# Performance work log

Measured on AMD Instinct MI355X. Metric: run time of the kernel, lower is better.

## Reference

```python
import jax, jax.numpy as jnp
import numpy as np

# 8-bit signed symmetric quantization grid (bit buffer in the module is set to 8 at runtime)
SAT_MAX = 127.0
SAT_MIN = -127.0


def _squant_stage(rn, re, un, ue, up_p, dn, de, dn_p):
    """One SQuant flip stage over the last axis (vectorized SQuant_func).

    For each row: e = sum(rounding_error); flip round(|e|) elements.
    If e < 0 (under-rounded overall) flip the highest-up-priority elements up,
    else flip the highest-down-priority elements down. The boundary (last,
    lowest-priority flipped) element gets a nonzero priority in the opposite
    direction so the next (coarser) stage can revert it — this reproduces the
    in-place priority update SQuant_func performs after zeroing priorities.
    All tensors have shape [..., K].
    """
    e_sum = jnp.sum(re, axis=-1)                                   # [...]
    n_flip = jnp.round(jnp.abs(e_sum)).astype(jnp.int32)[..., None]  # [...,1]
    flip_up = (e_sum < 0)[..., None]                               # [...,1]
    prio = jnp.where(flip_up, up_p, dn_p)
    order = jnp.argsort(-prio, axis=-1)        # descending priority
    rank = jnp.argsort(order, axis=-1)         # rank[i] = position of i in order
    mask = rank < n_flip                       # elements to flip
    rn2 = jnp.where(mask, jnp.where(flip_up, un, dn), rn)
    re2 = jnp.where(mask, jnp.where(flip_up, ue, de), re)
    # boundary element (rank == n_flip-1) gets opposite-direction priority
    boundary = mask & (rank == (n_flip - 1))
    b_prio = jnp.where(boundary, jnp.abs(re2), 0.0)
    up_p2 = jnp.where(flip_up, jnp.zeros_like(b_prio), b_prio)
    dn_p2 = jnp.where(flip_up, b_prio, jnp.zeros_like(b_prio))
    return rn2, re2, up_p2, dn_p2


def adaptive_round(x, t_min, t_max):
    rn = jnp.round(x)
    re = rn - x
    # up candidates: elements rounded down (re < 0) and not saturated high
    ue = jnp.where((x >= t_max) | (re > 0), 0.0, re)
    up_p = jnp.abs(ue)
    nz_u = ue != 0
    ue = jnp.where(nz_u, ue + 1.0, ue)
    un = jnp.where(nz_u, rn + 1.0, rn)
    # down candidates: elements rounded up (re > 0) and not saturated low
    de = jnp.where((x <= t_min) | (re < 0), 0.0, re)
    dn_p = jnp.abs(de)
    nz_d = de != 0
    de = jnp.where(nz_d, de - 1.0, de)
    dn = jnp.where(nz_d, rn - 1.0, rn)

    OC, IC = x.shape[0], x.shape[1]
    K = x.size // (OC * IC)
    shp_k = (OC, IC, K)         # squant-k: per (oc, ic) kernel row
    rn_k, re_k, up_p_k, dn_p_k = _squant_stage(
        rn.reshape(shp_k), re.reshape(shp_k),
        un.reshape(shp_k), ue.reshape(shp_k), up_p.reshape(shp_k),
        dn.reshape(shp_k), de.reshape(shp_k), dn_p.reshape(shp_k))
    shp_c = (1, OC, IC * K)     # squant-c: per oc channel row
    rn_c, _, _, _ = _squant_stage(
        rn_k.reshape(shp_c), re_k.reshape(shp_c),
        un.reshape(shp_c), ue.reshape(shp_c), up_p_k.reshape(shp_c),
        dn.reshape(shp_c), de.reshape(shp_c), dn_p_k.reshape(shp_c))
    return rn_c.reshape(x.shape)


def setup_inputs() -> dict:
    key = jax.random.key(0)
    tensor = jax.random.normal(key, (1024, 1024, 3, 3), dtype=jnp.float32)
    return {"tensor": tensor}


def reference(tensor) -> jnp.ndarray:
    # symmetric linear quantization params from tensor min/max (weight path)
    max_abs = jnp.maximum(jnp.abs(jnp.max(tensor)), jnp.abs(jnp.min(tensor)))
    scale = max_abs / SAT_MAX                       # element scale
    q = jnp.clip(tensor / scale, SAT_MIN, SAT_MAX)  # linear_quantize
    q = adaptive_round(q, SAT_MIN, SAT_MAX)         # SQuant adaptive rounding
    return q * scale                                # linear_dequantize
```

## Files before the change

### kernel.cpp

```cpp
#include <hip/hip_runtime.h>

#define OC 1024
#define ICN 1024
#define KK 9
#define NELEM (OC * ICN * KK)
#define CH (ICN * KK)
#define CH4 (CH / 4)
#define CHH (CH / 2)
#define CHH4 (CHH / 4)
#define BT 512
#define KMB 1024

__global__ void __launch_bounds__(256) kmax_part(const float* __restrict__ x,
                                                 float* __restrict__ part) {
    __shared__ float s_m[4];
    const int tid = blockIdx.x * 256 + threadIdx.x;
    const int stride = KMB * 256;
    const float4* x4 = (const float4*)x;
    float m = 0.f;
    #pragma unroll
    for (int k = 0; k < 9; ++k) {
        float4 v = x4[tid + k * stride];
        m = fmaxf(m, fmaxf(fmaxf(fabsf(v.x), fabsf(v.y)), fmaxf(fabsf(v.z), fabsf(v.w))));
    }
    #pragma unroll
    for (int off = 32; off > 0; off >>= 1)
        m = fmaxf(m, __shfl_xor(m, off, 64));
    if ((threadIdx.x & 63) == 0) s_m[threadIdx.x >> 6] = m;
    __syncthreads();
    if (threadIdx.x == 0)
        part[blockIdx.x] = fmaxf(fmaxf(s_m[0], s_m[1]), fmaxf(s_m[2], s_m[3]));
}

__global__ void __launch_bounds__(256) kmax_atomic(const float* __restrict__ x,
                                                   unsigned* __restrict__ ws) {
    __shared__ float s_m[4];
    const int tid = blockIdx.x * 256 + threadIdx.x;
    const int stride = KMB * 256;
    const float4* x4 = (const float4*)x;
    float m = 0.f;
    #pragma unroll
    for (int k = 0; k < 9; ++k) {
        float4 v = x4[tid + k * stride];
        m = fmaxf(m, fmaxf(fmaxf(fabsf(v.x), fabsf(v.y)), fmaxf(fabsf(v.z), fabsf(v.w))));
    }
    #pragma unroll
    for (int off = 32; off > 0; off >>= 1)
        m = fmaxf(m, __shfl_xor(m, off, 64));
    if ((threadIdx.x & 63) == 0) s_m[threadIdx.x >> 6] = m;
    __syncthreads();
    if (threadIdx.x == 0) {
        m = fmaxf(fmaxf(s_m[0], s_m[1]), fmaxf(s_m[2], s_m[3]));
        atomicMax(ws, __float_as_uint(m));
    }
}

template <int C>
__device__ __forceinline__ void red_step(unsigned& key, unsigned& row) {
    unsigned k2 = (unsigned)__builtin_amdgcn_update_dpp(0, (int)key, C, 0xF, 0xF, false);
    unsigned r2 = (unsigned)__builtin_amdgcn_update_dpp(0, (int)row, C, 0xF, 0xF, false);
    if (k2 >= key) { key = k2; row = r2; }
}

__device__ __forceinline__ void wave_argmax(unsigned& key, unsigned& row) {
    red_step<0x111>(key, row);
    red_step<0x112>(key, row);
    red_step<0x114>(key, row);
    red_step<0x118>(key, row);
    red_step<0x142>(key, row);
    red_step<0x143>(key, row);
}

__global__ void __launch_bounds__(BT, 8) squant_kernel(const float* __restrict__ x,
                                                       float* __restrict__ out,
                                                       const float* __restrict__ part,
                                                       int nparts) {
    __shared__ __align__(16) signed char s_q[CH];
    __shared__ __align__(16) float s_stage[CHH];
    __shared__ float s_res[ICN];
    __shared__ float s_prio[ICN];
    __shared__ int   s_meta[ICN];
    __shared__ float s_mx[8];

    const int oc = blockIdx.x;
    const int t  = threadIdx.x;
    const long long ocbase = (long long)oc * CH;

    float m;
    if (nparts > 0) {
        m = fmaxf(part[t], part[t + BT]);
        #pragma unroll
        for (int off = 32; off > 0; off >>= 1)
            m = fmaxf(m, __shfl_xor(m, off, 64));
        if ((t & 63) == 0) s_mx[t >> 6] = m;
    } else if (t == 0) {
        s_mx[0] = __uint_as_float(((const unsigned*)part)[0]);
    }
    __syncthreads();
    if (nparts > 0) {
        m = s_mx[0];
        #pragma unroll
        for (int w = 1; w < 8; ++w) m = fmaxf(m, s_mx[w]);
    } else {
        m = s_mx[0];
    }
    const float scale = m / 127.0f;
    const float iscale = 1.0f / scale;

    #pragma unroll
    for (int ph = 0; ph < 2; ++ph) {
        const int rowbase = ph * BT;
        const float4* src = (const float4*)(x + ocbase + (long long)rowbase * KK);
        float4* st4 = (float4*)s_stage;
        for (int i = t; i < CHH4; i += BT) st4[i] = src[i];
        __syncthreads();

        const int row = rowbase + t;
        const float* px = s_stage + t * KK;
        float rn[KK], re[KK];
        float e = 0.f;
        #pragma unroll
        for (int k = 0; k < KK; ++k) {
            float q = px[k] * iscale;
            q = fminf(fmaxf(q, -127.f), 127.f);
            float r = rintf(q);
            rn[k] = r;
            re[k] = r - q;
            e += re[k];
        }
        int nf = (int)rintf(fabsf(e));
        bool up = e < 0.f;
        unsigned flipped = 0u;
        int bidx = -1;
        float b_re = 0.f;
        for (int f = 0; f < nf; ++f) {
            float bp = 0.f; int bk = -1; float cre = 0.f;
            #pragma unroll
            for (int k = 0; k < KK; ++k) {
                bool cand = up ? (re[k] < 0.f) : (re[k] > 0.f);
                float p = (cand && !((flipped >> k) & 1u)) ? fabsf(re[k]) : 0.f;
                if (p > bp) { bp = p; bk = k; cre = re[k]; }
            }
            if (bk < 0) break;
            flipped |= (1u << bk);
            bidx = bk; b_re = cre;
        }
        int cnt = __popc(flipped);
        float sgn = up ? 1.f : -1.f;

        #pragma unroll
        for (int k = 0; k < KK; ++k) {
            float v = rn[k] + (((flipped >> k) & 1u) ? sgn : 0.f);
            s_q[row * KK + k] = (signed char)(int)v;
        }
        s_res[row] = e + sgn * (float)cnt;
        if (bidx >= 0) {
            s_prio[row] = fabsf(b_re + sgn);
            s_meta[row] = (row * KK + bidx) | ((up ? 1 : 0) << 16);
        } else {
            s_prio[row] = 0.f;
            s_meta[row] = 0;
        }
        __syncthreads();
    }

    if (t < 64) {
        float s = 0.f;
        #pragma unroll
        for (int i = 0; i < ICN / 64; ++i) s += s_res[t + i * 64];
        #pragma unroll
        for (int off = 32; off > 0; off >>= 1) s += __shfl_xor(s, off, 64);

        int n2 = (int)rintf(fabsf(s));
        bool up2 = s < 0.f;
        if (n2 > 0) {
            unsigned k[ICN / 64];
            #pragma unroll
            for (int i = 0; i < ICN / 64; ++i) {
                int r = t + i * 64;
                float pr = s_prio[r];
                int dir = s_meta[r] >> 16;
                bool match = ((dir != 0) != up2);
                unsigned bits = __float_as_uint(pr);
                k[i] = (pr > 0.f && match)
                         ? (((bits - 0x3F000000u + 1u) << 4) | (15u - (unsigned)i))
                         : 0u;
            }
            unsigned bk = 0u;
            #pragma unroll
            for (int i = 0; i < ICN / 64; ++i) bk = (k[i] > bk) ? k[i] : bk;
            unsigned brow = (unsigned)(t + (15 - (int)(bk & 15u)) * 64);

            unsigned fmask = 0u;
            int f = 0;
            for (; f < n2; ++f) {
                unsigned key = bk, row = brow;
                wave_argmax(key, row);
                unsigned kw = (unsigned)__builtin_amdgcn_readlane((int)key, 63);
                unsigned rw = (unsigned)__builtin_amdgcn_readlane((int)row, 63);
                if (kw == 0u) break;
                int iw = 15 - (int)(kw & 15u);
                bool owner = (t == (int)(rw & 63u));
                if (owner) fmask |= (1u << iw);
                unsigned zm = owner ? (1u << iw) : 0u;
                unsigned nb = 0u;
                #pragma unroll
                for (int i = 0; i < ICN / 64; ++i) {
                    unsigned ki = ((zm >> i) & 1u) ? 0u : k[i];
                    k[i] = ki;
                    nb = (ki > nb) ? ki : nb;
                }
                bk = nb;
                brow = (unsigned)(t + (15 - (int)(bk & 15u)) * 64);
            }

            #pragma unroll
            for (int i = 0; i < ICN / 64; ++i) {
                if ((fmask >> i) & 1u) {
                    int meta = s_meta[t + i * 64];
                    int gid = meta & 0xFFFF;
                    s_q[gid] = (signed char)(s_q[gid] + ((meta >> 16) ? -1 : 1));
                }
            }

            if (f < n2) {
                int remaining = n2 - f;
                if (remaining > CH) remaining = CH;
                for (int j = t; j < remaining; j += 64) {
                    float q = x[ocbase + j] * iscale;
                    q = fminf(fmaxf(q, -127.f), 127.f);
                    float r = rintf(q);
                    float rr = r - q;
                    float v = up2 ? ((rr < 0.f) ? r + 1.f : r)
                                  : ((rr > 0.f) ? r - 1.f : r);
                    s_q[j] = (signed char)(int)v;
                }
            }
        }
    }
    __syncthreads();

    const int* qw = (const int*)s_q;
    float4* o4 = (float4*)(out + ocbase);
    for (int i = t; i < CH4; i += BT) {
        int w = qw[i];
        float4 o;
        o.x = (float)((int)(signed char)(w       & 0xFF)) * scale;
        o.y = (float)((int)(signed char)((w >> 8) & 0xFF)) * scale;
        o.z = (float)((int)(signed char)((w >> 16) & 0xFF)) * scale;
        o.w = (float)((int)(signed char)((w >> 24) & 0xFF)) * scale;
        o4[i] = o;
    }
}

extern "C" void kernel_launch(void* const* d_in, const int* in_sizes, int n_in,
                              void* d_out, int out_size, void* d_ws, size_t ws_size,
                              hipStream_t stream) {
    const float* x = (const float*)d_in[0];
    float* out = (float*)d_out;
    if (ws_size >= KMB * sizeof(float)) {
        float* part = (float*)d_ws;
        kmax_part<<<KMB, 256, 0, stream>>>(x, part);
        squant_kernel<<<OC, BT, 0, stream>>>(x, out, part, KMB);
    } else {
        unsigned* wsmax = (unsigned*)d_ws;
        hipMemsetAsync(d_ws, 0, 4, stream);
        kmax_atomic<<<KMB, 256, 0, stream>>>(x, wsmax);
        squant_kernel<<<OC, BT, 0, stream>>>(x, out, (const float*)d_ws, 0);
    }
}
```

Measured before the change: 106.2 us.

## Load rows directly into registers and drop LDS staging and extra barriers

Each thread now loads its two 9-element rows straight from global memory into registers at kernel start, instead of staging each half through a shared-memory buffer with vectorized copies and barriers. The global max is reduced redundantly inside each wave over the partial maxima, which removes the shared-memory slot and a block barrier. This cuts LDS usage, which may raise occupancy, and issues the loads before the max reduction so their latency overlaps it. The cost is that the per-thread loads are strided scalar accesses (stride of 9 floats) rather than coalesced float4 copies, and register pressure goes up.

```diff
diff --git a/kernel.cpp b/kernel.cpp
--- a/kernel.cpp
+++ b/kernel.cpp
@@ -6,8 +6,6 @@
 #define NELEM (OC * ICN * KK)
 #define CH (ICN * KK)
 #define CH4 (CH / 4)
-#define CHH (CH / 2)
-#define CHH4 (CHH / 4)
 #define BT 512
 #define KMB 1024
 
@@ -76,52 +74,44 @@
                                                        const float* __restrict__ part,
                                                        int nparts) {
     __shared__ __align__(16) signed char s_q[CH];
-    __shared__ __align__(16) float s_stage[CHH];
     __shared__ float s_res[ICN];
     __shared__ float s_prio[ICN];
     __shared__ int   s_meta[ICN];
-    __shared__ float s_mx[8];
 
     const int oc = blockIdx.x;
     const int t  = threadIdx.x;
     const long long ocbase = (long long)oc * CH;
 
+    const float* p0 = x + ocbase + (long long)t * KK;
+    const float* p1 = p0 + (long long)BT * KK;
+    float a0[KK], a1[KK];
+    #pragma unroll
+    for (int k = 0; k < KK; ++k) a0[k] = p0[k];
+    #pragma unroll
+    for (int k = 0; k < KK; ++k) a1[k] = p1[k];
+
     float m;
     if (nparts > 0) {
-        m = fmaxf(part[t], part[t + BT]);
+        m = 0.f;
+        #pragma unroll
+        for (int i = 0; i < 16; ++i) m = fmaxf(m, part[(t & 63) + i * 64]);
         #pragma unroll
         for (int off = 32; off > 0; off >>= 1)
             m = fmaxf(m, __shfl_xor(m, off, 64));
-        if ((t & 63) == 0) s_mx[t >> 6] = m;
-    } else if (t == 0) {
-        s_mx[0] = __uint_as_float(((const unsigned*)part)[0]);
-    }
-    __syncthreads();
-    if (nparts > 0) {
-        m = s_mx[0];
-        #pragma unroll
-        for (int w = 1; w < 8; ++w) m = fmaxf(m, s_mx[w]);
     } else {
-        m = s_mx[0];
+        m = __uint_as_float(((const unsigned*)part)[0]);
     }
     const float scale = m / 127.0f;
     const float iscale = 1.0f / scale;
 
     #pragma unroll
-    for (int ph = 0; ph < 2; ++ph) {
-        const int rowbase = ph * BT;
-        const float4* src = (const float4*)(x + ocbase + (long long)rowbase * KK);
-        float4* st4 = (float4*)s_stage;
-        for (int i = t; i < CHH4; i += BT) st4[i] = src[i];
-        __syncthreads();
-
-        const int row = rowbase + t;
-        const float* px = s_stage + t * KK;
+    for (int half = 0; half < 2; ++half) {
+        const int row = t + half * BT;
         float rn[KK], re[KK];
         float e = 0.f;
         #pragma unroll
         for (int k = 0; k < KK; ++k) {
-            float q = px[k] * iscale;
+            float q = (half ? a1[k] : a0[k]) * iscale;
             q = fminf(fmaxf(q, -127.f), 127.f);
             float r = rintf(q);
             rn[k] = r;
@@ -161,8 +151,8 @@
             s_prio[row] = 0.f;
             s_meta[row] = 0;
         }
-        __syncthreads();
-    }
+    }
+    __syncthreads();
 
     if (t < 64) {
         float s = 0.f;
@@ -245,8 +235,8 @@
     for (int i = t; i < CH4; i += BT) {
         int w = qw[i];
         float4 o;
-        o.x = (float)((int)(signed char)(w       & 0xFF)) * scale;
-        o.y = (float)((int)(signed char)((w >> 8) & 0xFF)) * scale;
+        o.x = (float)((int)(signed char)(w        & 0xFF)) * scale;
+        o.y = (float)((int)(signed char)((w >> 8)  & 0xFF)) * scale;
         o.z = (float)((int)(signed char)((w >> 16) & 0xFF)) * scale;
         o.w = (float)((int)(signed char)((w >> 24) & 0xFF)) * scale;
         o4[i] = o;
```

New measurement: 104.2 us. No clear change (-1.8%).
